# Kernel optimization log

Measured on AMD Instinct MI355X. Metric: run time of the kernel, lower is better.

## Reference

```python
import jax, jax.numpy as jnp
import numpy as np

B, T, DIN, E, H, P = 8, 2048, 256, 256, 4, 8
HD = E // H


def _xavier(key, out_dim, in_dim):
    lim = float(np.sqrt(6.0 / (in_dim + out_dim)))
    return jax.random.uniform(key, (out_dim, in_dim), jnp.float32, -lim, lim)


def setup_inputs() -> dict:
    key = jax.random.key(0)
    ks = jax.random.split(key, 9)
    return {
        "x": jax.random.normal(ks[0], (B, T, DIN), jnp.float32),
        "w_in": _xavier(ks[1], E, DIN), "b_in": jnp.zeros((E,), jnp.float32),
        # MHA in-projections (torch packs qkv; xavier over packed [3E,E] approximated per-slice)
        "w_q": _xavier(ks[2], E, E), "b_q": jnp.zeros((E,), jnp.float32),
        "w_k": _xavier(ks[3], E, E), "b_k": jnp.zeros((E,), jnp.float32),
        "w_v": _xavier(ks[4], E, E), "b_v": jnp.zeros((E,), jnp.float32),
        "w_o": _xavier(ks[5], E, E), "b_o": jnp.zeros((E,), jnp.float32),
        "w_bd": _xavier(ks[6], 1, E), "b_bd": jnp.zeros((1,), jnp.float32),
        "w_pr": _xavier(ks[7], E, E), "b_pr": jnp.zeros((E,), jnp.float32),
    }


def reference(x, w_in, b_in, w_q, b_q, w_k, b_k, w_v, b_v, w_o, b_o, w_bd, b_bd, w_pr, b_pr):
    b, t, _ = x.shape
    h = x @ w_in.T + b_in                                   # [B,T,E]
    # self-attention (batch_first MHA, eval mode -> dropout is identity)
    q = (h @ w_q.T + b_q).reshape(b, t, H, HD)
    k = (h @ w_k.T + b_k).reshape(b, t, H, HD)
    v = (h @ w_v.T + b_v).reshape(b, t, H, HD)
    scale = 1.0 / np.sqrt(HD).astype(np.float32)
    scores = jnp.einsum("bqhd,bkhd->bhqk", q * scale, k)   # [B,H,T,T]
    attn = jax.nn.softmax(scores, axis=-1)
    ao = jnp.einsum("bhqk,bkhd->bqhd", attn, v).reshape(b, t, E)
    ao = ao @ w_o.T + b_o
    # boundary scoring -> dynamic patch ids
    bs = jax.nn.sigmoid(ao @ w_bd.T + b_bd)[..., 0]         # [B,T]
    cum = jnp.cumsum(bs, axis=1)
    normalized = cum / jnp.maximum(cum[:, -1:], 1e-6)
    pid = jnp.minimum((normalized * P).astype(jnp.int32), P - 1)  # [B,T]
    # mean-pool h into P dynamic patches (scatter_add + counts, via one-hot segment matmul)
    oh = jax.nn.one_hot(pid, P, dtype=h.dtype)              # [B,T,P]
    patch_emb = jnp.einsum("btp,btd->bpd", oh, h)           # [B,P,E]
    counts = oh.sum(axis=1)[..., None]                      # [B,P,1]
    patch_emb = patch_emb / jnp.maximum(counts, 1.0)
    return patch_emb @ w_pr.T + b_pr                        # [B,P,E]
```

## Files before the change

### kernel.cpp

```cpp
#include <hip/hip_runtime.h>
#include <cstddef>

#define NB 8
#define NT 2048
#define NE 256
#define NH 4
#define ND 64
#define NP 8

typedef short bf16x8 __attribute__((ext_vector_type(8)));
typedef float f32x4 __attribute__((ext_vector_type(4)));

__device__ __forceinline__ unsigned short f2bf(float f) {
  unsigned u = __builtin_bit_cast(unsigned, f);
  u += 0x7fffu + ((u >> 16) & 1u);
  return (unsigned short)(u >> 16);
}
__device__ __forceinline__ float bf2f(unsigned short h) {
  unsigned u = ((unsigned)h) << 16;
  return __builtin_bit_cast(float, u);
}
__device__ __forceinline__ void split2(float a, float b, unsigned& hi, unsigned& lo) {
  const unsigned short ha = f2bf(a), hb = f2bf(b);
  hi = (unsigned)ha | ((unsigned)hb << 16);
  const unsigned short la = f2bf(a - bf2f(ha));
  const unsigned short lb = f2bf(b - bf2f(hb));
  lo = (unsigned)la | ((unsigned)lb << 16);
}
__device__ __forceinline__ void gld16(const void* g, void* l) {
  __builtin_amdgcn_global_load_lds((const __attribute__((address_space(1))) unsigned*)g,
                                   (__attribute__((address_space(3))) unsigned*)l, 16, 0, 0);
}

#define QSC 0.180336880111120419f

__global__ __launch_bounds__(256) void setup_kernel(
    const float* __restrict__ w_in, const float* __restrict__ w_q,
    const float* __restrict__ w_k, const float* __restrict__ b_q,
    const float* __restrict__ b_k, const float* __restrict__ w_o,
    const float* __restrict__ b_o, const float* __restrict__ w_bd,
    const float* __restrict__ b_bd, const float* __restrict__ w_v,
    const float* __restrict__ b_v,
    unsigned short* __restrict__ wihi, unsigned short* __restrict__ wilo,
    unsigned short* __restrict__ wqkvhi, unsigned short* __restrict__ wqkvlo,
    float* __restrict__ bqk, float* __restrict__ consts, float* __restrict__ psum)
{
  __shared__ float wbd_s[NE];
  __shared__ float u_s[NE];
  const int b = blockIdx.x, tid = threadIdx.x;
  if (b < 512) {
    const int i = b * 256 + tid;
    const float v = (i < 65536) ? w_q[i] * QSC : w_k[i - 65536];
    const unsigned short h = f2bf(v);
    wqkvhi[i] = h;
    wqkvlo[i] = f2bf(v - bf2f(h));
    if (i < 512) bqk[i] = (i < 256) ? b_q[i] * QSC : b_k[i - 256];
  } else if (b < 576) {
    const int i = (b - 512) * 256 + tid;
    const float4 v = *(const float4*)(w_in + (size_t)i * 4);
    const float vv[4] = {v.x, v.y, v.z, v.w};
    unsigned short h4[4], l4[4];
    #pragma unroll
    for (int j = 0; j < 4; ++j) {
      h4[j] = f2bf(vv[j]);
      l4[j] = f2bf(vv[j] - bf2f(h4[j]));
    }
    *(ushort2*)(wihi + (size_t)i * 4)     = make_ushort2(h4[0], h4[1]);
    *(ushort2*)(wihi + (size_t)i * 4 + 2) = make_ushort2(h4[2], h4[3]);
    *(ushort2*)(wilo + (size_t)i * 4)     = make_ushort2(l4[0], l4[1]);
    *(ushort2*)(wilo + (size_t)i * 4 + 2) = make_ushort2(l4[2], l4[3]);
  } else if (b == 576) {
    wbd_s[tid] = w_bd[tid];
    __syncthreads();
    float a = 0.f;
    for (int j = 0; j < NE; ++j) a = fmaf(wbd_s[j], w_o[j * NE + tid], a);
    u_s[tid] = a;
    __syncthreads();
    #pragma unroll
    for (int hh = 0; hh < NH; ++hh) {
      float a2 = 0.f;
      for (int d = 0; d < ND; ++d)
        a2 = fmaf(u_s[hh * ND + d], w_v[(size_t)(hh * ND + d) * NE + tid], a2);
      const unsigned short hb = f2bf(a2);
      wqkvhi[(512 + hh) * 256 + tid] = hb;
      wqkvlo[(512 + hh) * 256 + tid] = f2bf(a2 - bf2f(hb));
    }
    for (int i = tid; i < 60 * 256; i += 256) {
      wqkvhi[516 * 256 + i] = 0;
      wqkvlo[516 * 256 + i] = 0;
    }
    if (tid == 0) {
      float cc = 0.f;
      for (int j = 0; j < NE; ++j) cc = fmaf(wbd_s[j], b_o[j], cc);
      consts[0] = cc + b_bd[0];
    }
    if (tid < 4) {
      float cv = 0.f;
      for (int d = 0; d < ND; ++d) cv = fmaf(u_s[tid * ND + d], b_v[tid * ND + d], cv);
      bqk[512 + tid] = cv;
    } else if (tid < 64) {
      bqk[512 + tid] = 0.f;
    }
  } else {
    for (int i = tid; i < NB * NP * NE; i += 256) psum[i] = 0.f;
  }
}

__global__ __launch_bounds__(256) void hgemm_kernel(
    const float* __restrict__ x,
    const unsigned short* __restrict__ wihi, const unsigned short* __restrict__ wilo,
    const float* __restrict__ b_in,
    unsigned short* __restrict__ hhi, unsigned short* __restrict__ hlo)
{
  __shared__ __align__(16) char sm[2][24576];
  const int tid = threadIdx.x;
  const int wave = tid >> 6, lane = tid & 63;
  const int lr = lane & 15, lg = lane >> 4;
  const int wm = wave >> 1, wn = wave & 1;
  const int bid = blockIdx.x;
  const int idx = bid >> 3;
  const int m0 = ((bid & 7) * 16 + (idx >> 2)) * 128;
  const int n0 = (idx & 3) * 64;

  const float* aSrc[4];
  #pragma unroll
  for (int c = 0; c < 4; ++c) {
    const int L = c * 4096 + tid * 16;
    const int row = L >> 7, w = (L >> 4) & 7;
    aSrc[c] = x + (size_t)(m0 + row) * 256 + (w ^ (row & 7)) * 4;
  }
  const unsigned short* wSrc[2];
  #pragma unroll
  for (int c = 0; c < 2; ++c) {
    const int L = c * 4096 + tid * 16;
    const int half = (L >> 12) & 1;
    const int Lh = L & 4095;
    const int col = Lh >> 6, w = (Lh >> 4) & 3;
    wSrc[c] = (half ? wilo : wihi) + (size_t)(n0 + col) * 256 + (w ^ ((col >> 1) & 3)) * 8;
  }
  int aoff[4][2], woff[2];
  #pragma unroll
  for (int s = 0; s < 4; ++s) {
    const int row = wm * 64 + s * 16 + lr;
    const int b0 = row * 128 + lg * 32;
    const int f = (row & 7) << 4;
    aoff[s][0] = b0 ^ f;
    aoff[s][1] = (b0 + 16) ^ f;
  }
  #pragma unroll
  for (int ns = 0; ns < 2; ++ns) {
    const int col = wn * 32 + ns * 16 + lr;
    woff[ns] = (col * 64 + lg * 16) ^ (((col >> 1) & 3) << 4);
  }

  f32x4 acc[4][2];
  #pragma unroll
  for (int s = 0; s < 4; ++s)
    #pragma unroll
    for (int ns = 0; ns < 2; ++ns) acc[s][ns] = (f32x4){0.f, 0.f, 0.f, 0.f};

  {
    char* lb = sm[0];
    #pragma unroll
    for (int c = 0; c < 4; ++c) gld16(aSrc[c], lb + c * 4096 + wave * 1024);
    #pragma unroll
    for (int c = 0; c < 2; ++c) gld16(wSrc[c], lb + 16384 + c * 4096 + wave * 1024);
  }

  for (int kt = 0; kt < 8; ++kt) {
    __syncthreads();
    if (kt < 7) {
      char* nb = sm[(kt + 1) & 1];
      #pragma unroll
      for (int c = 0; c < 4; ++c) gld16(aSrc[c] + (kt + 1) * 32, nb + c * 4096 + wave * 1024);
      #pragma unroll
      for (int c = 0; c < 2; ++c) gld16(wSrc[c] + (kt + 1) * 32, nb + 16384 + c * 4096 + wave * 1024);
    }
    const char* lb = sm[kt & 1];
    bf16x8 ah[4], al[4], wh[2], wl[2];
    #pragma unroll
    for (int s = 0; s < 4; ++s) {
      const f32x4 p0 = *(const f32x4*)(lb + aoff[s][0]);
      const f32x4 p1 = *(const f32x4*)(lb + aoff[s][1]);
      unsigned h0, h1, h2, h3, l0, l1, l2, l3;
      split2(p0[0], p0[1], h0, l0);
      split2(p0[2], p0[3], h1, l1);
      split2(p1[0], p1[1], h2, l2);
      split2(p1[2], p1[3], h3, l3);
      const uint4 hu = make_uint4(h0, h1, h2, h3);
      const uint4 lu = make_uint4(l0, l1, l2, l3);
      ah[s] = __builtin_bit_cast(bf16x8, hu);
      al[s] = __builtin_bit_cast(bf16x8, lu);
    }
    #pragma unroll
    for (int ns = 0; ns < 2; ++ns) {
      wh[ns] = *(const bf16x8*)(lb + 16384 + woff[ns]);
      wl[ns] = *(const bf16x8*)(lb + 20480 + woff[ns]);
    }
    #pragma unroll
    for (int s = 0; s < 4; ++s)
      #pragma unroll
      for (int ns = 0; ns < 2; ++ns) {
        acc[s][ns] = __builtin_amdgcn_mfma_f32_16x16x32_bf16(ah[s], wh[ns], acc[s][ns], 0, 0, 0);
        acc[s][ns] = __builtin_amdgcn_mfma_f32_16x16x32_bf16(ah[s], wl[ns], acc[s][ns], 0, 0, 0);
        acc[s][ns] = __builtin_amdgcn_mfma_f32_16x16x32_bf16(al[s], wh[ns], acc[s][ns], 0, 0, 0);
      }
  }
  #pragma unroll
  for (int s = 0; s < 4; ++s)
    #pragma unroll
    for (int ns = 0; ns < 2; ++ns)
      #pragma unroll
      for (int reg = 0; reg < 4; ++reg) {
        const int row = m0 + wm * 64 + s * 16 + lg * 4 + reg;
        const int col = n0 + wn * 32 + ns * 16 + lr;
        const float v = acc[s][ns][reg] + b_in[col];
        const size_t i2 = (size_t)row * 256 + col;
        const unsigned short hb = f2bf(v);
        hhi[i2] = hb;
        hlo[i2] = f2bf(v - bf2f(hb));
      }
}

__global__ __launch_bounds__(256) void qkvgemm_kernel(
    const unsigned short* __restrict__ Ahi, const unsigned short* __restrict__ Alo,
    const unsigned short* __restrict__ Whi, const unsigned short* __restrict__ Wlo,
    const float* __restrict__ bias,
    unsigned short* __restrict__ Qhi, unsigned short* __restrict__ Qlo,
    unsigned short* __restrict__ Khi, unsigned short* __restrict__ Klo,
    float* __restrict__ vubuf)
{
  __shared__ __align__(16) char sm[2][24576];
  const int tid = threadIdx.x;
  const int wave = tid >> 6, lane = tid & 63;
  const int lr = lane & 15, lg = lane >> 4;
  const int wm = wave >> 1, wn = wave & 1;
  const int bid = blockIdx.x;
  const int idx = bid >> 3;
  const int m0 = ((bid & 7) * 16 + idx / 9) * 128;
  const int n0 = (idx % 9) * 64;

  const unsigned short* aSrc[4];
  #pragma unroll
  for (int c = 0; c < 4; ++c) {
    const int L = c * 4096 + tid * 16;
    const int half = L >> 13;
    const int Lh = L & 8191;
    const int row = Lh >> 6, w = (Lh >> 4) & 3;
    aSrc[c] = (half ? Alo : Ahi) + (size_t)(m0 + row) * 256 + (w ^ ((row >> 1) & 3)) * 8;
  }
  const unsigned short* wSrc[2];
  #pragma unroll
  for (int c = 0; c < 2; ++c) {
    const int L = c * 4096 + tid * 16;
    const int half = (L >> 12) & 1;
    const int Lh = L & 4095;
    const int col = Lh >> 6, w = (Lh >> 4) & 3;
    wSrc[c] = (half ? Wlo : Whi) + (size_t)(n0 + col) * 256 + (w ^ ((col >> 1) & 3)) * 8;
  }
  int aoff[4], woff[2];
  #pragma unroll
  for (int s = 0; s < 4; ++s) {
    const int row = wm * 64 + s * 16 + lr;
    aoff[s] = (row * 64 + lg * 16) ^ (((row >> 1) & 3) << 4);
  }
  #pragma unroll
  for (int ns = 0; ns < 2; ++ns) {
    const int col = wn * 32 + ns * 16 + lr;
    woff[ns] = (col * 64 + lg * 16) ^ (((col >> 1) & 3) << 4);
  }

  f32x4 acc[4][2];
  #pragma unroll
  for (int s = 0; s < 4; ++s)
    #pragma unroll
    for (int ns = 0; ns < 2; ++ns) acc[s][ns] = (f32x4){0.f, 0.f, 0.f, 0.f};

  {
    char* lb = sm[0];
    #pragma unroll
    for (int c = 0; c < 4; ++c) gld16(aSrc[c], lb + c * 4096 + wave * 1024);
    #pragma unroll
    for (int c = 0; c < 2; ++c) gld16(wSrc[c], lb + 16384 + c * 4096 + wave * 1024);
  }

  for (int kt = 0; kt < 8; ++kt) {
    __syncthreads();
    if (kt < 7) {
      char* nb = sm[(kt + 1) & 1];
      #pragma unroll
      for (int c = 0; c < 4; ++c) gld16(aSrc[c] + (kt + 1) * 32, nb + c * 4096 + wave * 1024);
      #pragma unroll
      for (int c = 0; c < 2; ++c) gld16(wSrc[c] + (kt + 1) * 32, nb + 16384 + c * 4096 + wave * 1024);
    }
    const char* lb = sm[kt & 1];
    bf16x8 ah[4], al[4], wh[2], wl[2];
    #pragma unroll
    for (int s = 0; s < 4; ++s) {
      ah[s] = *(const bf16x8*)(lb + aoff[s]);
      al[s] = *(const bf16x8*)(lb + 8192 + aoff[s]);
    }
    #pragma unroll
    for (int ns = 0; ns < 2; ++ns) {
      wh[ns] = *(const bf16x8*)(lb + 16384 + woff[ns]);
      wl[ns] = *(const bf16x8*)(lb + 20480 + woff[ns]);
    }
    #pragma unroll
    for (int s = 0; s < 4; ++s)
      #pragma unroll
      for (int ns = 0; ns < 2; ++ns) {
        acc[s][ns] = __builtin_amdgcn_mfma_f32_16x16x32_bf16(ah[s], wh[ns], acc[s][ns], 0, 0, 0);
        acc[s][ns] = __builtin_amdgcn_mfma_f32_16x16x32_bf16(ah[s], wl[ns], acc[s][ns], 0, 0, 0);
        acc[s][ns] = __builtin_amdgcn_mfma_f32_16x16x32_bf16(al[s], wh[ns], acc[s][ns], 0, 0, 0);
      }
  }
  #pragma unroll
  for (int s = 0; s < 4; ++s)
    #pragma unroll
    for (int ns = 0; ns < 2; ++ns)
      #pragma unroll
      for (int reg = 0; reg < 4; ++reg) {
        const int row = m0 + wm * 64 + s * 16 + lg * 4 + reg;
        const int col = n0 + wn * 32 + ns * 16 + lr;
        const float v = acc[s][ns][reg] + bias[col];
        const int b = row >> 11, t = row & 2047;
        if (col < 512) {
          const int c = col & 255;
          const int head = c >> 6, d = c & 63;
          const size_t i2 = (((size_t)(b * NH + head)) * NT + t) * ND + d;
          const unsigned short hb = f2bf(v);
          if (col < 256) { Qhi[i2] = hb; Qlo[i2] = f2bf(v - bf2f(hb)); }
          else           { Khi[i2] = hb; Klo[i2] = f2bf(v - bf2f(hb)); }
        } else if (col < 516) {
          vubuf[((size_t)(b * NH + (col - 512))) * NT + t] = v;
        }
      }
}

__global__ __launch_bounds__(512) void attn_kernel6(
    const unsigned short* __restrict__ qhi, const unsigned short* __restrict__ qlo,
    const unsigned short* __restrict__ khi, const unsigned short* __restrict__ klo,
    const float* __restrict__ vu, float2* __restrict__ part2)
{
  __shared__ __align__(16) char kbuf[4][16384];
  __shared__ float vu_s[256];
  const int tid = threadIdx.x;
  const int wave = tid >> 6, lane = tid & 63;
  const int lr = lane & 15, lg = lane >> 4;
  const int bid = blockIdx.x;
  const int idx = bid >> 3;
  const int bh = (bid & 7) * 4 + (idx >> 6);
  const int rem = idx & 63;
  const int qt = rem >> 3, kh = rem & 7;
  const size_t base = (size_t)bh * NT * ND;
  const int qrow0 = qt * 256 + wave * 32;
  const int krow0 = kh * 256;

  if (tid < 256) vu_s[tid] = vu[(size_t)bh * NT + krow0 + tid];

  bf16x8 qf[2][2][2];
  #pragma unroll
  for (int s = 0; s < 2; ++s)
    #pragma unroll
    for (int ds = 0; ds < 2; ++ds) {
      const size_t off = base + (size_t)(qrow0 + s * 16 + lr) * ND + ds * 32 + lg * 8;
      qf[s][ds][0] = *(const bf16x8*)(qhi + off);
      qf[s][ds][1] = *(const bf16x8*)(qlo + off);
    }

  const int so = (tid * 16) ^ (((tid >> 3) & 7) << 4);
  int ro0[4], ro1[4];
  #pragma unroll
  for (int ns = 0; ns < 4; ++ns) {
    const int r = ns * 16 + lr;
    const int sw = (r & 7) << 4;
    const int ob = r * 128 + lg * 16;
    ro0[ns] = ob ^ sw;
    ro1[ns] = (ob + 64) ^ sw;
  }
  const char* srcH = (const char*)(khi + base + (size_t)krow0 * ND);
  const char* srcL = (const char*)(klo + base + (size_t)krow0 * ND);
  #pragma unroll
  for (int t = 0; t < 4; ++t) {
    gld16(srcH + t * 8192 + so, &kbuf[t][wave * 1024]);
    gld16(srcL + t * 8192 + so, &kbuf[t][8192 + wave * 1024]);
  }
  __syncthreads();

  float l[8], sv[8];
  #pragma unroll
  for (int i = 0; i < 8; ++i) { l[i] = 0.f; sv[i] = 0.f; }

  #pragma unroll 2
  for (int kt = 0; kt < 4; ++kt) {
    const char* kb = (const char*)kbuf[kt];
    f32x4 acc[2][4];
    float vuv[4];
    __builtin_amdgcn_s_setprio(1);
    #pragma unroll
    for (int ns = 0; ns < 4; ++ns) {
      const bf16x8 kh0 = *(const bf16x8*)(kb + ro0[ns]);
      const bf16x8 kh1 = *(const bf16x8*)(kb + ro1[ns]);
      const bf16x8 kl0 = *(const bf16x8*)(kb + 8192 + ro0[ns]);
      const bf16x8 kl1 = *(const bf16x8*)(kb + 8192 + ro1[ns]);
      vuv[ns] = vu_s[kt * 64 + ns * 16 + lr];
      #pragma unroll
      for (int s = 0; s < 2; ++s) {
        acc[s][ns] = (f32x4){0.f, 0.f, 0.f, 0.f};
        acc[s][ns] = __builtin_amdgcn_mfma_f32_16x16x32_bf16(qf[s][0][0], kh0, acc[s][ns], 0, 0, 0);
        acc[s][ns] = __builtin_amdgcn_mfma_f32_16x16x32_bf16(qf[s][0][0], kl0, acc[s][ns], 0, 0, 0);
        acc[s][ns] = __builtin_amdgcn_mfma_f32_16x16x32_bf16(qf[s][0][1], kh0, acc[s][ns], 0, 0, 0);
        acc[s][ns] = __builtin_amdgcn_mfma_f32_16x16x32_bf16(qf[s][1][0], kh1, acc[s][ns], 0, 0, 0);
        acc[s][ns] = __builtin_amdgcn_mfma_f32_16x16x32_bf16(qf[s][1][0], kl1, acc[s][ns], 0, 0, 0);
        acc[s][ns] = __builtin_amdgcn_mfma_f32_16x16x32_bf16(qf[s][1][1], kh1, acc[s][ns], 0, 0, 0);
      }
    }
    __builtin_amdgcn_s_setprio(0);
    #pragma unroll
    for (int s = 0; s < 2; ++s)
      #pragma unroll
      for (int reg = 0; reg < 4; ++reg) {
        const int ri = s * 4 + reg;
        #pragma unroll
        for (int ns = 0; ns < 4; ++ns) {
          const float e = __builtin_amdgcn_exp2f(acc[s][ns][reg]);
          l[ri] += e;
          sv[ri] = fmaf(e, vuv[ns], sv[ri]);
        }
      }
  }
  #pragma unroll
  for (int ri = 0; ri < 8; ++ri) {
    #pragma unroll
    for (int off = 1; off < 16; off <<= 1) {
      l[ri]  += __shfl_xor(l[ri],  off, 16);
      sv[ri] += __shfl_xor(sv[ri], off, 16);
    }
  }
  if (lr == 0) {
    #pragma unroll
    for (int s = 0; s < 2; ++s)
      #pragma unroll
      for (int reg = 0; reg < 4; ++reg) {
        const int row = qrow0 + s * 16 + lg * 4 + reg;
        part2[(((size_t)bh * NT + row) << 3) + kh] = make_float2(l[s * 4 + reg], sv[s * 4 + reg]);
      }
  }
}

__global__ __launch_bounds__(256) void boundary_kernel(
    const float4* __restrict__ part4, const float* __restrict__ consts,
    int* __restrict__ pid, int* __restrict__ counts)
{
  const int b = blockIdx.x, tid = threadIdx.x;
  __shared__ float partial[256];
  __shared__ int cnt_s[8];
  const float c = consts[0];
  float v[8];
  float run = 0.f;
  #pragma unroll
  for (int i = 0; i < 8; ++i) {
    const int t = tid * 8 + i;
    float logit = c;
    #pragma unroll
    for (int hh = 0; hh < NH; ++hh) {
      const size_t p0 = ((size_t)(b * NH + hh) * NT + t) * 4;
      float lsum = 0.f, ssum = 0.f;
      #pragma unroll
      for (int q = 0; q < 4; ++q) {
        const float4 p = part4[p0 + q];
        lsum += p.x + p.z;
        ssum += p.y + p.w;
      }
      logit += ssum / lsum;
    }
    const float bs = 1.f / (1.f + expf(-logit));
    run += bs;
    v[i] = run;
  }
  float x = run;
  partial[tid] = x;
  __syncthreads();
  for (int off = 1; off < 256; off <<= 1) {
    const float y = (tid >= off) ? partial[tid - off] : 0.f;
    __syncthreads();
    x += y;
    partial[tid] = x;
    __syncthreads();
  }
  const float total = partial[255];
  if (tid < 8) cnt_s[tid] = 0;
  __syncthreads();
  const float denom = fmaxf(total, 1e-6f);
  const float excl = x - run;
  #pragma unroll
  for (int i = 0; i < 8; ++i) {
    const float norm = (excl + v[i]) / denom;
    int pp = (int)(norm * 8.f);
    pp = pp > 7 ? 7 : pp;
    pid[b * NT + tid * 8 + i] = pp;
    atomicAdd(&cnt_s[pp], 1);
  }
  __syncthreads();
  if (tid < 8) counts[b * 8 + tid] = cnt_s[tid];
}

__global__ __launch_bounds__(256) void pool_kernel(
    const unsigned short* __restrict__ hhi, const int* __restrict__ pid,
    float* __restrict__ psum)
{
  const int b = blockIdx.x >> 4, chunk = blockIdx.x & 15;
  const int tid = threadIdx.x;
  __shared__ int pid_s[128];
  const int t0 = chunk * 128;
  if (tid < 128) pid_s[tid] = pid[b * NT + t0 + tid];
  __syncthreads();
  float acc[8] = {};
  for (int tok = 0; tok < 128; ++tok) {
    const float val = bf2f(hhi[((size_t)b * NT + t0 + tok) * NE + tid]);
    const int p = pid_s[tok];
    #pragma unroll
    for (int pp = 0; pp < 8; ++pp) acc[pp] += (p == pp) ? val : 0.f;
  }
  #pragma unroll
  for (int pp = 0; pp < 8; ++pp)
    atomicAdd(&psum[((size_t)b * NP + pp) * NE + tid], acc[pp]);
}

__global__ __launch_bounds__(256) void final_kernel(
    const float* __restrict__ psum, const int* __restrict__ counts,
    const float* __restrict__ w_pr, const float* __restrict__ b_pr, float* __restrict__ out)
{
  const int bp = blockIdx.x;
  const int tid = threadIdx.x;
  __shared__ float pe[NE];
  const float cnt = fmaxf((float)counts[bp], 1.f);
  pe[tid] = psum[(size_t)bp * NE + tid] / cnt;
  __syncthreads();
  float acc = 0.f;
  for (int e = 0; e < NE; ++e) acc = fmaf(pe[e], w_pr[(size_t)tid * NE + e], acc);
  out[(size_t)bp * NE + tid] = acc + b_pr[tid];
}

extern "C" void kernel_launch(void* const* d_in, const int* in_sizes, int n_in,
                              void* d_out, int out_size, void* d_ws, size_t ws_size,
                              hipStream_t stream) {
  (void)in_sizes; (void)n_in; (void)out_size; (void)ws_size;
  const float* x    = (const float*)d_in[0];
  const float* w_in = (const float*)d_in[1];
  const float* b_in = (const float*)d_in[2];
  const float* w_q  = (const float*)d_in[3];
  const float* b_q  = (const float*)d_in[4];
  const float* w_k  = (const float*)d_in[5];
  const float* b_k  = (const float*)d_in[6];
  const float* w_v  = (const float*)d_in[7];
  const float* b_v  = (const float*)d_in[8];
  const float* w_o  = (const float*)d_in[9];
  const float* b_o  = (const float*)d_in[10];
  const float* w_bd = (const float*)d_in[11];
  const float* b_bd = (const float*)d_in[12];
  const float* w_pr = (const float*)d_in[13];
  const float* b_pr = (const float*)d_in[14];
  float* out = (float*)d_out;

  const size_t M = (size_t)NB * NT;
  unsigned short* hhi = (unsigned short*)d_ws;
  unsigned short* hlo = hhi + M * NE;
  unsigned short* qhi = hlo + M * NE;
  unsigned short* qlo = qhi + M * NE;
  unsigned short* khi = qlo + M * NE;
  unsigned short* klo = khi + M * NE;
  unsigned short* wihi = klo + M * NE;
  unsigned short* wilo = wihi + 65536;
  unsigned short* wqkvhi = wilo + 65536;
  unsigned short* wqkvlo = wqkvhi + 147456;
  float* bqk    = (float*)(wqkvlo + 147456);
  float* vubuf  = bqk + 576;
  float* part   = vubuf + 65536;
  float* consts = part + 1048576;
  float* psum   = consts + 8;
  int*   pid    = (int*)(psum + 16384);
  int*   counts = pid + 16384;

  setup_kernel<<<578, 256, 0, stream>>>(w_in, w_q, w_k, b_q, b_k, w_o, b_o,
      w_bd, b_bd, w_v, b_v, wihi, wilo, wqkvhi, wqkvlo, bqk, consts, psum);
  hgemm_kernel<<<512, 256, 0, stream>>>(x, wihi, wilo, b_in, hhi, hlo);
  qkvgemm_kernel<<<1152, 256, 0, stream>>>(hhi, hlo, wqkvhi, wqkvlo, bqk,
      qhi, qlo, khi, klo, vubuf);
  attn_kernel6<<<2048, 512, 0, stream>>>(qhi, qlo, khi, klo, vubuf, (float2*)part);
  boundary_kernel<<<8, 256, 0, stream>>>((const float4*)part, consts, pid, counts);
  pool_kernel<<<128, 256, 0, stream>>>(hhi, pid, psum);
  final_kernel<<<64, 256, 0, stream>>>(psum, counts, w_pr, b_pr, out);
}
```

Before: 166.4 us.

## Shrink attention tiles to 128x128 and split partial-sum combine into parallel kernel

The attention kernel now uses 128-query by 128-key tiles with 16 rows per wave instead of 256x256 with 32 rows per wave. This quadruples the grid to 8192 blocks, halves LDS use and adds a min-blocks launch bound, all aimed at raising occupancy. The per-row partial sums doubled to 16 key chunks, so a new 64-block combine kernel computes the sigmoid boundary scores in parallel, and the 8-block boundary kernel now only scans. The cost is more Q reloads and block launches, twice the partial-buffer traffic, and one extra kernel launch.

```diff
diff --git a/kernel.cpp b/kernel.cpp
--- a/kernel.cpp
+++ b/kernel.cpp
@@ -337,36 +337,34 @@
       }
 }
 
-__global__ __launch_bounds__(512) void attn_kernel6(
+__global__ __launch_bounds__(512, 6) void attn_kernel7(
     const unsigned short* __restrict__ qhi, const unsigned short* __restrict__ qlo,
     const unsigned short* __restrict__ khi, const unsigned short* __restrict__ klo,
     const float* __restrict__ vu, float2* __restrict__ part2)
 {
-  __shared__ __align__(16) char kbuf[4][16384];
-  __shared__ float vu_s[256];
+  __shared__ __align__(16) char kbuf[2][16384];
+  __shared__ float vu_s[128];
   const int tid = threadIdx.x;
   const int wave = tid >> 6, lane = tid & 63;
   const int lr = lane & 15, lg = lane >> 4;
   const int bid = blockIdx.x;
   const int idx = bid >> 3;
-  const int bh = (bid & 7) * 4 + (idx >> 6);
-  const int rem = idx & 63;
-  const int qt = rem >> 3, kh = rem & 7;
+  const int bh = (bid & 7) * 4 + (idx >> 8);
+  const int rem = idx & 255;
+  const int qt = rem >> 4, kh = rem & 15;
   const size_t base = (size_t)bh * NT * ND;
-  const int qrow0 = qt * 256 + wave * 32;
-  const int krow0 = kh * 256;
-
-  if (tid < 256) vu_s[tid] = vu[(size_t)bh * NT + krow0 + tid];
-
-  bf16x8 qf[2][2][2];
-  #pragma unroll
-  for (int s = 0; s < 2; ++s)
-    #pragma unroll
-    for (int ds = 0; ds < 2; ++ds) {
-      const size_t off = base + (size_t)(qrow0 + s * 16 + lr) * ND + ds * 32 + lg * 8;
-      qf[s][ds][0] = *(const bf16x8*)(qhi + off);
-      qf[s][ds][1] = *(const bf16x8*)(qlo + off);
-    }
+  const int qrow0 = qt * 128 + wave * 16;
+  const int krow0 = kh * 128;
+
+  if (tid < 128) vu_s[tid] = vu[(size_t)bh * NT + krow0 + tid];
+
+  bf16x8 qf[2][2];
+  #pragma unroll
+  for (int ds = 0; ds < 2; ++ds) {
+    const size_t off = base + (size_t)(qrow0 + lr) * ND + ds * 32 + lg * 8;
+    qf[ds][0] = *(const bf16x8*)(qhi + off);
+    qf[ds][1] = *(const bf16x8*)(qlo + off);
+  }
 
   const int so = (tid * 16) ^ (((tid >> 3) & 7) << 4);
   int ro0[4], ro1[4];
@@ -381,20 +379,21 @@
   const char* srcH = (const char*)(khi + base + (size_t)krow0 * ND);
   const char* srcL = (const char*)(klo + base + (size_t)krow0 * ND);
   #pragma unroll
-  for (int t = 0; t < 4; ++t) {
+  for (int t = 0; t < 2; ++t) {
     gld16(srcH + t * 8192 + so, &kbuf[t][wave * 1024]);
     gld16(srcL + t * 8192 + so, &kbuf[t][8192 + wave * 1024]);
   }
   __syncthreads();
 
-  float l[8], sv[8];
-  #pragma unroll
-  for (int i = 0; i < 8; ++i) { l[i] = 0.f; sv[i] = 0.f; }
-
-  #pragma unroll 2
-  for (int kt = 0; kt < 4; ++kt) {
+  float l[4], sv[4];
+  #pragma unroll
+  for (int i = 0; i < 4; ++i) { l[i] = 0.f; sv[i] = 0.f; }
+  const f32x4 Z = (f32x4){0.f, 0.f, 0.f, 0.f};
+
+  #pragma unroll
+  for (int kt = 0; kt < 2; ++kt) {
     const char* kb = (const char*)kbuf[kt];
-    f32x4 acc[2][4];
+    f32x4 acc[4];
     float vuv[4];
     __builtin_amdgcn_s_setprio(1);
     #pragma unroll
@@ -404,80 +403,75 @@
       const bf16x8 kl0 = *(const bf16x8*)(kb + 8192 + ro0[ns]);
       const bf16x8 kl1 = *(const bf16x8*)(kb + 8192 + ro1[ns]);
       vuv[ns] = vu_s[kt * 64 + ns * 16 + lr];
-      #pragma unroll
-      for (int s = 0; s < 2; ++s) {
-        acc[s][ns] = (f32x4){0.f, 0.f, 0.f, 0.f};
-        acc[s][ns] = __builtin_amdgcn_mfma_f32_16x16x32_bf16(qf[s][0][0], kh0, acc[s][ns], 0, 0, 0);
-        acc[s][ns] = __builtin_amdgcn_mfma_f32_16x16x32_bf16(qf[s][0][0], kl0, acc[s][ns], 0, 0, 0);
-        acc[s][ns] = __builtin_amdgcn_mfma_f32_16x16x32_bf16(qf[s][0][1], kh0, acc[s][ns], 0, 0, 0);
-        acc[s][ns] = __builtin_amdgcn_mfma_f32_16x16x32_bf16(qf[s][1][0], kh1, acc[s][ns], 0, 0, 0);
-        acc[s][ns] = __builtin_amdgcn_mfma_f32_16x16x32_bf16(qf[s][1][0], kl1, acc[s][ns], 0, 0, 0);
-        acc[s][ns] = __builtin_amdgcn_mfma_f32_16x16x32_bf16(qf[s][1][1], kh1, acc[s][ns], 0, 0, 0);
+      acc[ns] = __builtin_amdgcn_mfma_f32_16x16x32_bf16(qf[0][0], kh0, Z, 0, 0, 0);
+      acc[ns] = __builtin_amdgcn_mfma_f32_16x16x32_bf16(qf[0][0], kl0, acc[ns], 0, 0, 0);
+      acc[ns] = __builtin_amdgcn_mfma_f32_16x16x32_bf16(qf[0][1], kh0, acc[ns], 0, 0, 0);
+      acc[ns] = __builtin_amdgcn_mfma_f32_16x16x32_bf16(qf[1][0], kh1, acc[ns], 0, 0, 0);
+      acc[ns] = __builtin_amdgcn_mfma_f32_16x16x32_bf16(qf[1][0], kl1, acc[ns], 0, 0, 0);
+      acc[ns] = __builtin_amdgcn_mfma_f32_16x16x32_bf16(qf[1][1], kh1, acc[ns], 0, 0, 0);
+    }
+    __builtin_amdgcn_s_setprio(0);
+    #pragma unroll
+    for (int reg = 0; reg < 4; ++reg)
+      #pragma unroll
+      for (int ns = 0; ns < 4; ++ns) {
+        const float e = __builtin_amdgcn_exp2f(acc[ns][reg]);
+        l[reg] += e;
+        sv[reg] = fmaf(e, vuv[ns], sv[reg]);
       }
-    }
-    __builtin_amdgcn_s_setprio(0);
-    #pragma unroll
-    for (int s = 0; s < 2; ++s)
-      #pragma unroll
-      for (int reg = 0; reg < 4; ++reg) {
-        const int ri = s * 4 + reg;
-        #pragma unroll
-        for (int ns = 0; ns < 4; ++ns) {
-          const float e = __builtin_amdgcn_exp2f(acc[s][ns][reg]);
-          l[ri] += e;
-          sv[ri] = fmaf(e, vuv[ns], sv[ri]);
-        }
-      }
-  }
-  #pragma unroll
-  for (int ri = 0; ri < 8; ++ri) {
+  }
+  #pragma unroll
+  for (int reg = 0; reg < 4; ++reg) {
     #pragma unroll
     for (int off = 1; off < 16; off <<= 1) {
-      l[ri]  += __shfl_xor(l[ri],  off, 16);
-      sv[ri] += __shfl_xor(sv[ri], off, 16);
+      l[reg]  += __shfl_xor(l[reg],  off, 16);
+      sv[reg] += __shfl_xor(sv[reg], off, 16);
     }
   }
   if (lr == 0) {
     #pragma unroll
-    for (int s = 0; s < 2; ++s)
-      #pragma unroll
-      for (int reg = 0; reg < 4; ++reg) {
-        const int row = qrow0 + s * 16 + lg * 4 + reg;
-        part2[(((size_t)bh * NT + row) << 3) + kh] = make_float2(l[s * 4 + reg], sv[s * 4 + reg]);
-      }
-  }
+    for (int reg = 0; reg < 4; ++reg) {
+      const int row = qrow0 + lg * 4 + reg;
+      part2[(((size_t)bh * NT + row) << 4) + kh] = make_float2(l[reg], sv[reg]);
+    }
+  }
+}
+
+__global__ __launch_bounds__(256) void combine_kernel(
+    const float4* __restrict__ part4, const float* __restrict__ consts,
+    float* __restrict__ bs)
+{
+  const int gid = blockIdx.x * 256 + threadIdx.x;
+  const int b = gid >> 11, t = gid & 2047;
+  float logit = consts[0];
+  #pragma unroll
+  for (int hh = 0; hh < NH; ++hh) {
+    const size_t p0 = ((size_t)((b * NH + hh) * NT) + t) * 8;
+    float lsum = 0.f, ssum = 0.f;
+    #pragma unroll
+    for (int q = 0; q < 8; ++q) {
+      const float4 p = part4[p0 + q];
+      lsum += p.x + p.z;
+      ssum += p.y + p.w;
+    }
+    logit += ssum / lsum;
+  }
+  bs[gid] = 1.f / (1.f + expf(-logit));
 }
 
 __global__ __launch_bounds__(256) void boundary_kernel(
-    const float4* __restrict__ part4, const float* __restrict__ consts,
-    int* __restrict__ pid, int* __restrict__ counts)
+    const float* __restrict__ bs, int* __restrict__ pid, int* __restrict__ counts)
 {
   const int b = blockIdx.x, tid = threadIdx.x;
   __shared__ float partial[256];
   __shared__ int cnt_s[8];
-  const float c = consts[0];
   float v[8];
   float run = 0.f;
-  #pragma unroll
-  for (int i = 0; i < 8; ++i) {
-    const int t = tid * 8 + i;
-    float logit = c;
-    #pragma unroll
-    for (int hh = 0; hh < NH; ++hh) {
-      const size_t p0 = ((size_t)(b * NH + hh) * NT + t) * 4;
-      float lsum = 0.f, ssum = 0.f;
-      #pragma unroll
-      for (int q = 0; q < 4; ++q) {
-        const float4 p = part4[p0 + q];
-        lsum += p.x + p.z;
-        ssum += p.y + p.w;
-      }
-      logit += ssum / lsum;
-    }
-    const float bs = 1.f / (1.f + expf(-logit));
-    run += bs;
-    v[i] = run;
-  }
+  const float4 b0 = *(const float4*)(bs + b * NT + tid * 8);
+  const float4 b1 = *(const float4*)(bs + b * NT + tid * 8 + 4);
+  const float bv[8] = {b0.x, b0.y, b0.z, b0.w, b1.x, b1.y, b1.z, b1.w};
+  #pragma unroll
+  for (int i = 0; i < 8; ++i) { run += bv[i]; v[i] = run; }
   float x = run;
   partial[tid] = x;
   __syncthreads();
@@ -577,7 +571,8 @@
   float* bqk    = (float*)(wqkvlo + 147456);
   float* vubuf  = bqk + 576;
   float* part   = vubuf + 65536;
-  float* consts = part + 1048576;
+  float* bsbuf  = part + 2097152;
+  float* consts = bsbuf + 16384;
   float* psum   = consts + 8;
   int*   pid    = (int*)(psum + 16384);
   int*   counts = pid + 16384;
@@ -587,8 +582,9 @@
   hgemm_kernel<<<512, 256, 0, stream>>>(x, wihi, wilo, b_in, hhi, hlo);
   qkvgemm_kernel<<<1152, 256, 0, stream>>>(hhi, hlo, wqkvhi, wqkvlo, bqk,
       qhi, qlo, khi, klo, vubuf);
-  attn_kernel6<<<2048, 512, 0, stream>>>(qhi, qlo, khi, klo, vubuf, (float2*)part);
-  boundary_kernel<<<8, 256, 0, stream>>>((const float4*)part, consts, pid, counts);
+  attn_kernel7<<<8192, 512, 0, stream>>>(qhi, qlo, khi, klo, vubuf, (float2*)part);
+  combine_kernel<<<64, 256, 0, stream>>>((const float4*)part, consts, bsbuf);
+  boundary_kernel<<<8, 256, 0, stream>>>(bsbuf, pid, counts);
   pool_kernel<<<128, 256, 0, stream>>>(hhi, pid, psum);
   final_kernel<<<64, 256, 0, stream>>>(psum, counts, w_pr, b_pr, out);
 }
```

After: 168.8 us. About the same (+1.5%).

## Split boundary combine into parallel kernel and stagger attention K-tile order per wave

Applied to the files above, without the earlier changes.

The per-token reduction of attention partials (sum of exp and weighted values per head, then sigmoid) moves out of the 8-block boundary kernel into a new 64-block combine kernel that writes boundary scores to a buffer. The boundary kernel then only does the scan over those scores. This spreads the partial-buffer reads across many more threads. The attention kernel now fully unrolls its K-tile loop, staggers the starting tile by wave index to spread LDS bank accesses, and feeds a zero constant into the first MFMA instead of clearing the accumulator. The cost is one extra kernel launch and an extra global round trip for the scores.

```diff
diff --git a/kernel.cpp b/kernel.cpp
--- a/kernel.cpp
+++ b/kernel.cpp
@@ -337,7 +337,7 @@
       }
 }
 
-__global__ __launch_bounds__(512) void attn_kernel6(
+__global__ __launch_bounds__(512) void attn_kernel8(
     const unsigned short* __restrict__ qhi, const unsigned short* __restrict__ qlo,
     const unsigned short* __restrict__ khi, const unsigned short* __restrict__ klo,
     const float* __restrict__ vu, float2* __restrict__ part2)
@@ -390,9 +390,11 @@
   float l[8], sv[8];
   #pragma unroll
   for (int i = 0; i < 8; ++i) { l[i] = 0.f; sv[i] = 0.f; }
-
-  #pragma unroll 2
-  for (int kt = 0; kt < 4; ++kt) {
+  const f32x4 Z = (f32x4){0.f, 0.f, 0.f, 0.f};
+
+  #pragma unroll
+  for (int it = 0; it < 4; ++it) {
+    const int kt = (it + wave) & 3;
     const char* kb = (const char*)kbuf[kt];
     f32x4 acc[2][4];
     float vuv[4];
@@ -406,8 +408,7 @@
       vuv[ns] = vu_s[kt * 64 + ns * 16 + lr];
       #pragma unroll
       for (int s = 0; s < 2; ++s) {
-        acc[s][ns] = (f32x4){0.f, 0.f, 0.f, 0.f};
-        acc[s][ns] = __builtin_amdgcn_mfma_f32_16x16x32_bf16(qf[s][0][0], kh0, acc[s][ns], 0, 0, 0);
+        acc[s][ns] = __builtin_amdgcn_mfma_f32_16x16x32_bf16(qf[s][0][0], kh0, Z, 0, 0, 0);
         acc[s][ns] = __builtin_amdgcn_mfma_f32_16x16x32_bf16(qf[s][0][0], kl0, acc[s][ns], 0, 0, 0);
         acc[s][ns] = __builtin_amdgcn_mfma_f32_16x16x32_bf16(qf[s][0][1], kh0, acc[s][ns], 0, 0, 0);
         acc[s][ns] = __builtin_amdgcn_mfma_f32_16x16x32_bf16(qf[s][1][0], kh1, acc[s][ns], 0, 0, 0);
@@ -448,36 +449,41 @@
   }
 }
 
+__global__ __launch_bounds__(256) void combine_kernel(
+    const float4* __restrict__ part4, const float* __restrict__ consts,
+    float* __restrict__ bs)
+{
+  const int gid = blockIdx.x * 256 + threadIdx.x;
+  const int b = gid >> 11, t = gid & 2047;
+  float logit = consts[0];
+  #pragma unroll
+  for (int hh = 0; hh < NH; ++hh) {
+    const size_t p0 = ((size_t)((b * NH + hh) * NT) + t) * 4;
+    float lsum = 0.f, ssum = 0.f;
+    #pragma unroll
+    for (int q = 0; q < 4; ++q) {
+      const float4 p = part4[p0 + q];
+      lsum += p.x + p.z;
+      ssum += p.y + p.w;
+    }
+    logit += ssum / lsum;
+  }
+  bs[gid] = 1.f / (1.f + expf(-logit));
+}
+
 __global__ __launch_bounds__(256) void boundary_kernel(
-    const float4* __restrict__ part4, const float* __restrict__ consts,
-    int* __restrict__ pid, int* __restrict__ counts)
+    const float* __restrict__ bs, int* __restrict__ pid, int* __restrict__ counts)
 {
   const int b = blockIdx.x, tid = threadIdx.x;
   __shared__ float partial[256];
   __shared__ int cnt_s[8];
-  const float c = consts[0];
   float v[8];
   float run = 0.f;
-  #pragma unroll
-  for (int i = 0; i < 8; ++i) {
-    const int t = tid * 8 + i;
-    float logit = c;
-    #pragma unroll
-    for (int hh = 0; hh < NH; ++hh) {
-      const size_t p0 = ((size_t)(b * NH + hh) * NT + t) * 4;
-      float lsum = 0.f, ssum = 0.f;
-      #pragma unroll
-      for (int q = 0; q < 4; ++q) {
-        const float4 p = part4[p0 + q];
-        lsum += p.x + p.z;
-        ssum += p.y + p.w;
-      }
-      logit += ssum / lsum;
-    }
-    const float bs = 1.f / (1.f + expf(-logit));
-    run += bs;
-    v[i] = run;
-  }
+  const float4 b0 = *(const float4*)(bs + b * NT + tid * 8);
+  const float4 b1 = *(const float4*)(bs + b * NT + tid * 8 + 4);
+  const float bv[8] = {b0.x, b0.y, b0.z, b0.w, b1.x, b1.y, b1.z, b1.w};
+  #pragma unroll
+  for (int i = 0; i < 8; ++i) { run += bv[i]; v[i] = run; }
   float x = run;
   partial[tid] = x;
   __syncthreads();
@@ -577,7 +583,8 @@
   float* bqk    = (float*)(wqkvlo + 147456);
   float* vubuf  = bqk + 576;
   float* part   = vubuf + 65536;
-  float* consts = part + 1048576;
+  float* bsbuf  = part + 1048576;
+  float* consts = bsbuf + 16384;
   float* psum   = consts + 8;
   int*   pid    = (int*)(psum + 16384);
   int*   counts = pid + 16384;
@@ -587,8 +594,9 @@
   hgemm_kernel<<<512, 256, 0, stream>>>(x, wihi, wilo, b_in, hhi, hlo);
   qkvgemm_kernel<<<1152, 256, 0, stream>>>(hhi, hlo, wqkvhi, wqkvlo, bqk,
       qhi, qlo, khi, klo, vubuf);
-  attn_kernel6<<<2048, 512, 0, stream>>>(qhi, qlo, khi, klo, vubuf, (float2*)part);
-  boundary_kernel<<<8, 256, 0, stream>>>((const float4*)part, consts, pid, counts);
+  attn_kernel8<<<2048, 512, 0, stream>>>(qhi, qlo, khi, klo, vubuf, (float2*)part);
+  combine_kernel<<<64, 256, 0, stream>>>((const float4*)part, consts, bsbuf);
+  boundary_kernel<<<8, 256, 0, stream>>>(bsbuf, pid, counts);
   pool_kernel<<<128, 256, 0, stream>>>(hhi, pid, psum);
   final_kernel<<<64, 256, 0, stream>>>(psum, counts, w_pr, b_pr, out);
 }
```

New measurement: 154.1 us (median of 2 runs). 1.08x faster.
